# Optimization experiments

Measured on AMD Instinct MI355X. Metric: run time of the kernel, lower is better.

## Reference

```python
import jax, jax.numpy as jnp
import numpy as np

NEG = -1e9

def mask_from_lens(src_lens, lip_lens, Tx, Ty):
    # [B, Tx, Ty] valid mask
    mx = jnp.arange(Tx)[None, :] < src_lens[:, None]
    my = jnp.arange(Ty)[None, :] < lip_lens[:, None]
    return (mx[:, :, None] & my[:, None, :]).astype(jnp.float32)

def maximum_path(value, mask):
    # Monotonic alignment search (VITS-style). value, mask: [B, Tx, Ty]
    B, Tx, Ty = value.shape
    value = value * mask
    xr = jnp.arange(Tx)[None, :]

    def fwd(v, inp):
        val_j, j = inp
        v0 = jnp.concatenate([jnp.full((B, 1), NEG, value.dtype), v[:, :-1]], axis=1)
        stay = v >= v0                      # True: best prev is same x
        vmax = jnp.where(stay, v, v0)
        vnew = jnp.where(xr <= j, vmax + val_j, NEG)
        return vnew, stay

    val_T = jnp.transpose(value, (2, 0, 1))          # [Ty,B,Tx]
    _, dirs = jax.lax.scan(fwd, jnp.zeros((B, Tx), value.dtype),
                           (val_T, jnp.arange(Ty)))
    mask_T = jnp.transpose(mask, (2, 0, 1)) > 0
    dirs = jnp.where(mask_T, dirs, True)             # padded cols: stay

    idx0 = mask[:, :, 0].sum(1).astype(jnp.int32) - 1  # src_lens - 1
    br = jnp.arange(B)

    def bwd(index, dir_j):
        onehot = jax.nn.one_hot(index, Tx, dtype=value.dtype)
        d = dir_j[br, index]
        return index + d.astype(jnp.int32) - 1, onehot

    _, path = jax.lax.scan(bwd, idx0, dirs, reverse=True)  # [Ty,B,Tx]
    return jnp.transpose(path, (1, 2, 0)) * mask

def setup_inputs() -> dict:
    key = jax.random.key(0)
    k1, k2, k3, k4, k5 = jax.random.split(key, 5)
    B, Ts, Tl, D = 32, 512, 2048, 256
    lip_motion_embedding = jax.random.normal(k1, (B, Tl, D), jnp.float32)
    output_phoneme = jax.random.normal(k2, (B, Ts, D), jnp.float32)
    src_lens = jax.random.randint(k3, (B,), Ts // 2, Ts + 1, jnp.int32)
    lip_lens = jax.random.randint(k4, (B,), Tl // 2, Tl + 1, jnp.int32)
    d_targets = jax.random.randint(k5, (B, Ts), 1, 8, jnp.int32)
    d_targets = jnp.where(jnp.arange(Ts)[None, :] < src_lens[:, None], d_targets, 0)
    return {"lip_motion_embedding": lip_motion_embedding,
            "output_phoneme": output_phoneme,
            "d_targets": d_targets,
            "src_lens": src_lens,
            "lip_lens": lip_lens}

def reference(lip_motion_embedding, output_phoneme, d_targets, src_lens, lip_lens):
    B, Tl, D = lip_motion_embedding.shape
    Ts = output_phoneme.shape[1]

    # mean expansion coefficient
    mean_cof = (d_targets.sum(-1) / lip_lens).mean()

    # normalized similarity  [B, Ts, Tl]
    norm_lip = lip_motion_embedding / jnp.linalg.norm(lip_motion_embedding, axis=2, keepdims=True)
    text_norm_base = jnp.linalg.norm(output_phoneme, axis=2, keepdims=True)
    norm_text = jnp.nan_to_num(output_phoneme / (text_norm_base + 1), nan=1.0)
    similarity = jnp.einsum('bld,bsd->bsl', norm_lip, norm_text)

    # duration targets rescaled to lip frame rate
    cofs = d_targets.sum(1) / lip_lens                      # [B]
    lip_targets = jnp.round(d_targets / cofs[:, None])      # [B, Ts] float
    dif = lip_lens.astype(lip_targets.dtype) - lip_targets.sum(1)
    max_idx = jnp.argmax(lip_targets, axis=1)
    lip_targets = lip_targets.at[jnp.arange(B), max_idx].add(dif)

    # gt_similarity: contiguous segments of ones per phoneme (vectorized scatter)
    lt = lip_targets.astype(jnp.int32)
    ends = jnp.cumsum(lt, axis=1)                           # [B, Ts]
    begins = ends - lt
    kk = jnp.arange(Tl)[None, None, :]
    gt_similarity = ((kk >= begins[:, :, None]) & (kk < ends[:, :, None])).astype(similarity.dtype)

    mask_sim = mask_from_lens(src_lens, lip_lens, Ts, Tl)
    alignment = maximum_path(similarity, mask_sim)
    d_predictions = jax.lax.stop_gradient(alignment.sum(-1)) * mean_cof

    return similarity, gt_similarity, alignment, d_predictions
```

## Files before the change

kernel.cpp:

```cpp
#include <hip/hip_runtime.h>
#include <math.h>

#define BATCH 32
#define TS    512
#define TL    2048
#define DD    256
#define NEGV  -1e9f

#define SIM_OFF   ((size_t)0)
#define GT_OFF    ((size_t)BATCH*TS*TL)
#define ALIGN_OFF ((size_t)2*BATCH*TS*TL)
#define DPRED_OFF ((size_t)3*BATCH*TS*TL)

#define WS_MEAN   0
#define WS_COF    256
#define WS_LSCALE 512
#define WS_TSCALE 262656
#define WS_BEGIN  328192
#define WS_END    393728
#define WS_START2 459264
#define WS_END2   524800
#define WS_DIRS   590848

__global__ __launch_bounds__(256) void norm_kernel(const float* __restrict__ lip,
                                                   const float* __restrict__ phon,
                                                   float* __restrict__ lip_scale,
                                                   float* __restrict__ text_scale) {
    const int wave = threadIdx.x >> 6, lane = threadIdx.x & 63;
    const int row = blockIdx.x * 4 + wave;
    const int NL = BATCH * TL;
    const float* src = (row < NL) ? (lip + (size_t)row * DD)
                                  : (phon + (size_t)(row - NL) * DD);
    float4 q = *(const float4*)(src + lane * 4);
    float ss = q.x*q.x + q.y*q.y + q.z*q.z + q.w*q.w;
    #pragma unroll
    for (int off = 32; off; off >>= 1) ss += __shfl_xor(ss, off);
    if (lane == 0) {
        if (row < NL) lip_scale[row] = 1.0f / sqrtf(ss);
        else          text_scale[row - NL] = 1.0f / (sqrtf(ss) + 1.0f);
    }
}

__global__ __launch_bounds__(512) void prep_kernel(const int* __restrict__ d_targets,
                                                   const int* __restrict__ lip_lens,
                                                   int* __restrict__ begins,
                                                   int* __restrict__ ends,
                                                   float* __restrict__ cof_arr) {
    __shared__ int   si[512];
    __shared__ float sf[512];
    __shared__ int   sx[512];
    const int b = blockIdx.x, t = threadIdx.x;
    const int d = d_targets[b * TS + t];
    const int lipL = lip_lens[b];

    si[t] = d; __syncthreads();
    for (int off = 256; off; off >>= 1) { if (t < off) si[t] += si[t + off]; __syncthreads(); }
    const int sum_d = si[0]; __syncthreads();

    const float cofv = (float)sum_d / (float)lipL;
    float lt = rintf((float)d / cofv);

    sf[t] = lt; __syncthreads();
    for (int off = 256; off; off >>= 1) { if (t < off) sf[t] += sf[t + off]; __syncthreads(); }
    const float sumlt = sf[0]; __syncthreads();
    const float dif = (float)lipL - sumlt;

    sf[t] = lt; sx[t] = t; __syncthreads();
    for (int off = 256; off; off >>= 1) {
        if (t < off) {
            float v2 = sf[t + off]; int i2 = sx[t + off];
            if (v2 > sf[t] || (v2 == sf[t] && i2 < sx[t])) { sf[t] = v2; sx[t] = i2; }
        }
        __syncthreads();
    }
    const int max_idx = sx[0]; __syncthreads();
    if (t == max_idx) lt += dif;
    const int li = (int)lt;

    si[t] = li; __syncthreads();
    for (int off = 1; off < 512; off <<= 1) {
        int add = (t >= off) ? si[t - off] : 0;
        __syncthreads();
        si[t] += add;
        __syncthreads();
    }
    const int e = si[t];
    begins[b * TS + t] = e - li;
    ends[b * TS + t]   = e;
    if (t == 0) cof_arr[b] = cofv;
}

__global__ __launch_bounds__(256) void gemm_kernel(const float* __restrict__ lip,
                                                   const float* __restrict__ phon,
                                                   const float* __restrict__ lip_scale,
                                                   const float* __restrict__ text_scale,
                                                   const int* __restrict__ begins,
                                                   const int* __restrict__ ends,
                                                   float* __restrict__ sim,
                                                   float* __restrict__ gt) {
    const int b = blockIdx.z, tm = blockIdx.y, tn = blockIdx.x;
    const int t = threadIdx.x;
    __shared__ __align__(16) float As[16][132];
    __shared__ __align__(16) float Bs[16][132];

    const int r = t >> 1, sub = t & 1;
    const int tx = t & 15, ty = t >> 4;

    const float* Ag = phon + ((size_t)(b * TS + tm * 128 + r)) * DD + sub * 8;
    const float* Bg = lip  + ((size_t)(b * TL + tn * 128 + r)) * DD + sub * 8;
    const float sA = text_scale[b * TS + tm * 128 + r];
    const float sB = lip_scale[b * TL + tn * 128 + r];

    float4 ra0 = *(const float4*)(Ag);
    float4 ra1 = *(const float4*)(Ag + 4);
    float4 rb0 = *(const float4*)(Bg);
    float4 rb1 = *(const float4*)(Bg + 4);

    float acc[8][8];
    #pragma unroll
    for (int i = 0; i < 8; ++i)
        #pragma unroll
        for (int j = 0; j < 8; ++j) acc[i][j] = 0.0f;

    for (int kt = 0; kt < 16; ++kt) {
        __syncthreads();
        {
            const float* pa0 = &ra0.x; const float* pa1 = &ra1.x;
            const float* pb0 = &rb0.x; const float* pb1 = &rb1.x;
            #pragma unroll
            for (int kk = 0; kk < 4; ++kk) {
                As[sub * 8 + kk][r]     = pa0[kk] * sA;
                As[sub * 8 + 4 + kk][r] = pa1[kk] * sA;
                Bs[sub * 8 + kk][r]     = pb0[kk] * sB;
                Bs[sub * 8 + 4 + kk][r] = pb1[kk] * sB;
            }
        }
        __syncthreads();
        if (kt < 15) {
            ra0 = *(const float4*)(Ag + (kt + 1) * 16);
            ra1 = *(const float4*)(Ag + (kt + 1) * 16 + 4);
            rb0 = *(const float4*)(Bg + (kt + 1) * 16);
            rb1 = *(const float4*)(Bg + (kt + 1) * 16 + 4);
        }
        #pragma unroll
        for (int kk = 0; kk < 16; ++kk) {
            float4 t0 = *(const float4*)&As[kk][ty * 4];
            float4 t1 = *(const float4*)&As[kk][64 + ty * 4];
            float4 t2 = *(const float4*)&Bs[kk][tx * 4];
            float4 t3 = *(const float4*)&Bs[kk][64 + tx * 4];
            float a[8] = {t0.x, t0.y, t0.z, t0.w, t1.x, t1.y, t1.z, t1.w};
            float bb[8] = {t2.x, t2.y, t2.z, t2.w, t3.x, t3.y, t3.z, t3.w};
            #pragma unroll
            for (int i = 0; i < 8; ++i)
                #pragma unroll
                for (int j = 0; j < 8; ++j)
                    acc[i][j] = fmaf(a[i], bb[j], acc[i][j]);
        }
    }

    const size_t base = (size_t)b * TS * TL;
    #pragma unroll
    for (int mi = 0; mi < 2; ++mi) {
        #pragma unroll
        for (int im = 0; im < 4; ++im) {
            const int srow = tm * 128 + mi * 64 + ty * 4 + im;
            const int ai = mi * 4 + im;
            float* prow = sim + base + (size_t)srow * TL + tn * 128;
            float4 w0 = {acc[ai][0], acc[ai][1], acc[ai][2], acc[ai][3]};
            float4 w1 = {acc[ai][4], acc[ai][5], acc[ai][6], acc[ai][7]};
            *(float4*)(prow + tx * 4) = w0;
            *(float4*)(prow + 64 + tx * 4) = w1;

            const int bg = begins[b * TS + srow], en = ends[b * TS + srow];
            const int l0 = tn * 128 + tx * 4;
            float4 g0, g1;
            g0.x = (l0 + 0 >= bg && l0 + 0 < en) ? 1.f : 0.f;
            g0.y = (l0 + 1 >= bg && l0 + 1 < en) ? 1.f : 0.f;
            g0.z = (l0 + 2 >= bg && l0 + 2 < en) ? 1.f : 0.f;
            g0.w = (l0 + 3 >= bg && l0 + 3 < en) ? 1.f : 0.f;
            g1.x = (l0 + 64 >= bg && l0 + 64 < en) ? 1.f : 0.f;
            g1.y = (l0 + 65 >= bg && l0 + 65 < en) ? 1.f : 0.f;
            g1.z = (l0 + 66 >= bg && l0 + 66 < en) ? 1.f : 0.f;
            g1.w = (l0 + 67 >= bg && l0 + 67 < en) ? 1.f : 0.f;
            float* grow = gt + base + (size_t)srow * TL + tn * 128;
            *(float4*)(grow + tx * 4) = g0;
            *(float4*)(grow + 64 + tx * 4) = g1;
        }
    }
}

__device__ __forceinline__ void load8(float4 (&buf)[8][2], const float* simb, int L, int jb) {
    #pragma unroll
    for (int i = 0; i < 8; ++i) {
        const float* p = simb + (size_t)(L * 8 + i) * TL + jb;
        buf[i][0] = *(const float4*)p;
        buf[i][1] = *(const float4*)(p + 4);
    }
}

template <bool CHK>
__device__ __forceinline__ void step8(float4 (&buf)[8][2], int jb, float (&v)[8],
                                      unsigned (&w)[8], const float (&xm)[8], int L) {
    #pragma unroll
    for (int s = 0; s < 8; ++s) {
        const int j = jb + s;
        float up = __shfl_up(v[7], 1);
        if (L == 0) up = NEGV;
        #pragma unroll
        for (int i = 7; i >= 0; --i) {
            const float v0 = (i == 0) ? up : v[i - 1];
            const unsigned stay = (v[i] >= v0) ? 1u : 0u;
            const float vm = fmaxf(v[i], v0);
            const float va = ((const float*)&buf[i][0])[s];
            float nv = fmaf(va, xm[i], vm);
            if (CHK) nv = ((L * 8 + i) <= j) ? nv : NEGV;
            w[i] = w[i] * 2u + stay;
            v[i] = nv;
        }
    }
}

__global__ __launch_bounds__(64) void dp_kernel(const float* __restrict__ sim,
                                                const int* __restrict__ src_lens,
                                                const int* __restrict__ lip_lens,
                                                const float* __restrict__ cof_arr,
                                                float* __restrict__ mean_out,
                                                unsigned* __restrict__ dirs,
                                                int* __restrict__ start2,
                                                int* __restrict__ end2) {
    const int b = blockIdx.x, L = threadIdx.x;
    if (b == 0 && L == 0) {
        float s = 0.f;
        for (int i = 0; i < BATCH; ++i) s += cof_arr[i];
        mean_out[0] = s / 32.0f;
    }
    const int srcL = src_lens[b], lipL = lip_lens[b];
    const float* simb = sim + (size_t)b * TS * TL;

    float v[8]; unsigned w[8]; float xm[8];
    #pragma unroll
    for (int i = 0; i < 8; ++i) {
        v[i] = 0.f; w[i] = 0u;
        xm[i] = (L * 8 + i < srcL) ? 1.f : 0.f;
    }
    float4 bufA[8][2], bufB[8][2];
    const int jmax = (lipL + 31) & ~31;

    load8(bufA, simb, L, 0);
    for (int jb = 0; jb < jmax; jb += 16) {
        load8(bufB, simb, L, jb + 8);
        if (jb < 512) step8<true>(bufA, jb, v, w, xm, L);
        else          step8<false>(bufA, jb, v, w, xm, L);
        if ((jb & 31) == 24) {
            #pragma unroll
            for (int i = 0; i < 8; ++i) {
                dirs[((size_t)b * TS + L * 8 + i) * 64 + (jb >> 5)] = w[i];
                w[i] = 0u;
            }
        }
        if (jb + 16 < jmax) load8(bufA, simb, L, jb + 16);
        if (jb + 8 < 512) step8<true>(bufB, jb + 8, v, w, xm, L);
        else              step8<false>(bufB, jb + 8, v, w, xm, L);
        if (((jb + 8) & 31) == 24) {
            #pragma unroll
            for (int i = 0; i < 8; ++i) {
                dirs[((size_t)b * TS + L * 8 + i) * 64 + ((jb + 8) >> 5)] = w[i];
                w[i] = 0u;
            }
        }
    }

    #pragma unroll
    for (int i = 0; i < 8; ++i) {
        start2[b * TS + L + i * 64] = 0;
        end2[b * TS + L + i * 64] = 0;
    }
    asm volatile("s_waitcnt vmcnt(0)" ::: "memory");

    int x = srcL - 1;
    if (L == 0) end2[b * TS + x] = lipL;
    int j = lipL - 1;
    while (x > 0 && j >= 0) {
        const unsigned W = dirs[((size_t)b * TS + x) * 64 + (j >> 5)];
        const int jj = j & 31;
        const unsigned m = (~W) & (0xFFFFFFFFu << (31 - jj));
        if (m == 0u) { j -= jj + 1; continue; }
        const int jp = __builtin_ctz(m);
        const int jprime = (j & ~31) + (31 - jp);
        if (L == 0) { start2[b * TS + x] = jprime; end2[b * TS + x - 1] = jprime; }
        x -= 1; j = jprime - 1;
    }
}

__global__ __launch_bounds__(256) void align_kernel(const int* __restrict__ start2,
                                                    const int* __restrict__ end2,
                                                    const float* __restrict__ mean_cof,
                                                    float* __restrict__ alignOut,
                                                    float* __restrict__ dpred) {
    const int s = blockIdx.x, b = blockIdx.y, t = threadIdx.x;
    const int st = start2[b * TS + s], en = end2[b * TS + s];
    float* row = alignOut + ((size_t)b * TS + s) * TL;
    const int l0 = t * 8;
    float4 r0, r1;
    r0.x = (l0 + 0 >= st && l0 + 0 < en) ? 1.f : 0.f;
    r0.y = (l0 + 1 >= st && l0 + 1 < en) ? 1.f : 0.f;
    r0.z = (l0 + 2 >= st && l0 + 2 < en) ? 1.f : 0.f;
    r0.w = (l0 + 3 >= st && l0 + 3 < en) ? 1.f : 0.f;
    r1.x = (l0 + 4 >= st && l0 + 4 < en) ? 1.f : 0.f;
    r1.y = (l0 + 5 >= st && l0 + 5 < en) ? 1.f : 0.f;
    r1.z = (l0 + 6 >= st && l0 + 6 < en) ? 1.f : 0.f;
    r1.w = (l0 + 7 >= st && l0 + 7 < en) ? 1.f : 0.f;
    *(float4*)(row + l0) = r0;
    *(float4*)(row + l0 + 4) = r1;
    if (t == 0) dpred[b * TS + s] = (float)(en - st) * mean_cof[0];
}

extern "C" void kernel_launch(void* const* d_in, const int* in_sizes, int n_in,
                              void* d_out, int out_size, void* d_ws, size_t ws_size,
                              hipStream_t stream) {
    const float* lip   = (const float*)d_in[0];
    const float* phon  = (const float*)d_in[1];
    const int* d_tg    = (const int*)d_in[2];
    const int* src_l   = (const int*)d_in[3];
    const int* lip_l   = (const int*)d_in[4];
    float* out = (float*)d_out;

    char* ws = (char*)d_ws;
    float*    mean_cof   = (float*)(ws + WS_MEAN);
    float*    cof_arr    = (float*)(ws + WS_COF);
    float*    lip_scale  = (float*)(ws + WS_LSCALE);
    float*    text_scale = (float*)(ws + WS_TSCALE);
    int*      begins     = (int*)(ws + WS_BEGIN);
    int*      ends       = (int*)(ws + WS_END);
    int*      start2     = (int*)(ws + WS_START2);
    int*      end2       = (int*)(ws + WS_END2);
    unsigned* dirs       = (unsigned*)(ws + WS_DIRS);

    float* sim   = out + SIM_OFF;
    float* gt    = out + GT_OFF;
    float* aln   = out + ALIGN_OFF;
    float* dpred = out + DPRED_OFF;

    norm_kernel<<<(BATCH * TL + BATCH * TS) / 4, 256, 0, stream>>>(lip, phon, lip_scale, text_scale);
    prep_kernel<<<BATCH, 512, 0, stream>>>(d_tg, lip_l, begins, ends, cof_arr);
    gemm_kernel<<<dim3(TL / 128, TS / 128, BATCH), 256, 0, stream>>>(lip, phon, lip_scale, text_scale,
                                                                     begins, ends, sim, gt);
    dp_kernel<<<BATCH, 64, 0, stream>>>(sim, src_l, lip_l, cof_arr, mean_cof, dirs, start2, end2);
    align_kernel<<<dim3(TS, BATCH), 256, 0, stream>>>(start2, end2, mean_cof, aln, dpred);
}
```

Before: 1.189 ms.

## Write transposed similarity from GEMM so DP kernel reads contiguous column slices

The GEMM epilogue also writes a transposed copy of the similarity tile into the alignment output buffer, used as scratch. The DP kernel now reads that transposed layout, so each step's 64 lanes load one contiguous 2 KB row instead of 512 strided rows. This targets the latency-bound, poorly coalesced loads of the serial DP scan, which runs on only 32 blocks. The cost is an extra 128 MB write in the GEMM with strided scatter stores, and the approach depends on align_kernel fully overwriting the alignment buffer afterwards.

```diff
diff --git a/kernel.cpp b/kernel.cpp
--- a/kernel.cpp
+++ b/kernel.cpp
@@ -97,7 +97,8 @@
                                                    const int* __restrict__ begins,
                                                    const int* __restrict__ ends,
                                                    float* __restrict__ sim,
-                                                   float* __restrict__ gt) {
+                                                   float* __restrict__ gt,
+                                                   float* __restrict__ simT) {
     const int b = blockIdx.z, tm = blockIdx.y, tn = blockIdx.x;
     const int t = threadIdx.x;
     __shared__ __align__(16) float As[16][132];
@@ -187,32 +188,45 @@
             *(float4*)(grow + 64 + tx * 4) = g1;
         }
     }
-}
-
-__device__ __forceinline__ void load8(float4 (&buf)[8][2], const float* simb, int L, int jb) {
-    #pragma unroll
-    for (int i = 0; i < 8; ++i) {
-        const float* p = simb + (size_t)(L * 8 + i) * TL + jb;
-        buf[i][0] = *(const float4*)p;
-        buf[i][1] = *(const float4*)(p + 4);
+
+    {
+        float* tb = simT + (size_t)b * TL * TS + (size_t)(tn * 128) * TS + tm * 128;
+        #pragma unroll
+        for (int bj = 0; bj < 8; ++bj) {
+            const int lloc = (bj < 4) ? (tx * 4 + bj) : (64 + tx * 4 + (bj - 4));
+            float* trow = tb + (size_t)lloc * TS;
+            float4 w0 = {acc[0][bj], acc[1][bj], acc[2][bj], acc[3][bj]};
+            float4 w1 = {acc[4][bj], acc[5][bj], acc[6][bj], acc[7][bj]};
+            *(float4*)(trow + ty * 4) = w0;
+            *(float4*)(trow + 64 + ty * 4) = w1;
+        }
+    }
+}
+
+__device__ __forceinline__ void load8T(float4 (&buf)[8][2], const float* simTb, int L, int jb) {
+    #pragma unroll
+    for (int s = 0; s < 8; ++s) {
+        const float* p = simTb + (size_t)(jb + s) * TS + L * 8;
+        buf[s][0] = *(const float4*)p;
+        buf[s][1] = *(const float4*)(p + 4);
     }
 }
 
 template <bool CHK>
-__device__ __forceinline__ void step8(float4 (&buf)[8][2], int jb, float (&v)[8],
-                                      unsigned (&w)[8], const float (&xm)[8], int L) {
+__device__ __forceinline__ void step8T(float4 (&buf)[8][2], int jb, float (&v)[8],
+                                       unsigned (&w)[8], const float (&xm)[8], int L) {
     #pragma unroll
     for (int s = 0; s < 8; ++s) {
         const int j = jb + s;
         float up = __shfl_up(v[7], 1);
         if (L == 0) up = NEGV;
+        const float* vals = (const float*)&buf[s][0];
         #pragma unroll
         for (int i = 7; i >= 0; --i) {
             const float v0 = (i == 0) ? up : v[i - 1];
             const unsigned stay = (v[i] >= v0) ? 1u : 0u;
             const float vm = fmaxf(v[i], v0);
-            const float va = ((const float*)&buf[i][0])[s];
-            float nv = fmaf(va, xm[i], vm);
+            float nv = fmaf(vals[i], xm[i], vm);
             if (CHK) nv = ((L * 8 + i) <= j) ? nv : NEGV;
             w[i] = w[i] * 2u + stay;
             v[i] = nv;
@@ -220,7 +234,7 @@
     }
 }
 
-__global__ __launch_bounds__(64) void dp_kernel(const float* __restrict__ sim,
+__global__ __launch_bounds__(64) void dp_kernel(const float* __restrict__ simT,
                                                 const int* __restrict__ src_lens,
                                                 const int* __restrict__ lip_lens,
                                                 const float* __restrict__ cof_arr,
@@ -235,7 +249,7 @@
         mean_out[0] = s / 32.0f;
     }
     const int srcL = src_lens[b], lipL = lip_lens[b];
-    const float* simb = sim + (size_t)b * TS * TL;
+    const float* simTb = simT + (size_t)b * TL * TS;
 
     float v[8]; unsigned w[8]; float xm[8];
     #pragma unroll
@@ -246,11 +260,11 @@
     float4 bufA[8][2], bufB[8][2];
     const int jmax = (lipL + 31) & ~31;
 
-    load8(bufA, simb, L, 0);
+    load8T(bufA, simTb, L, 0);
     for (int jb = 0; jb < jmax; jb += 16) {
-        load8(bufB, simb, L, jb + 8);
-        if (jb < 512) step8<true>(bufA, jb, v, w, xm, L);
-        else          step8<false>(bufA, jb, v, w, xm, L);
+        load8T(bufB, simTb, L, jb + 8);
+        if (jb < 512) step8T<true>(bufA, jb, v, w, xm, L);
+        else          step8T<false>(bufA, jb, v, w, xm, L);
         if ((jb & 31) == 24) {
             #pragma unroll
             for (int i = 0; i < 8; ++i) {
@@ -258,9 +272,9 @@
                 w[i] = 0u;
             }
         }
-        if (jb + 16 < jmax) load8(bufA, simb, L, jb + 16);
-        if (jb + 8 < 512) step8<true>(bufB, jb + 8, v, w, xm, L);
-        else              step8<false>(bufB, jb + 8, v, w, xm, L);
+        if (jb + 16 < jmax) load8T(bufA, simTb, L, jb + 16);
+        if (jb + 8 < 512) step8T<true>(bufB, jb + 8, v, w, xm, L);
+        else              step8T<false>(bufB, jb + 8, v, w, xm, L);
         if (((jb + 8) & 31) == 24) {
             #pragma unroll
             for (int i = 0; i < 8; ++i) {
@@ -344,7 +358,7 @@
     norm_kernel<<<(BATCH * TL + BATCH * TS) / 4, 256, 0, stream>>>(lip, phon, lip_scale, text_scale);
     prep_kernel<<<BATCH, 512, 0, stream>>>(d_tg, lip_l, begins, ends, cof_arr);
     gemm_kernel<<<dim3(TL / 128, TS / 128, BATCH), 256, 0, stream>>>(lip, phon, lip_scale, text_scale,
-                                                                     begins, ends, sim, gt);
-    dp_kernel<<<BATCH, 64, 0, stream>>>(sim, src_l, lip_l, cof_arr, mean_cof, dirs, start2, end2);
+                                                                     begins, ends, sim, gt, aln);
+    dp_kernel<<<BATCH, 64, 0, stream>>>(aln, src_l, lip_l, cof_arr, mean_cof, dirs, start2, end2);
     align_kernel<<<dim3(TS, BATCH), 256, 0, stream>>>(start2, end2, mean_cof, aln, dpred);
 }
```

After: 1.138 ms. 4.3% less time.
